# Kernel optimization log

Measured on AMD Instinct MI355X. Metric: run time of the kernel, lower is better.

Reference implementation:

```python
import jax, jax.numpy as jnp
import numpy as np

N = 100_000      # nodes
E = 1_600_000    # edges
G = 256          # graphs in batch
FIN = 128


def setup_inputs() -> dict:
    key = jax.random.key(0)
    ks = jax.random.split(key, 12)
    inp = {
        "x": jax.random.normal(ks[0], (N, FIN), dtype=jnp.float32),
        "edge_index": jax.random.randint(ks[1], (2, E), 0, N),
        "batch": jnp.sort(jax.random.randint(ks[2], (N,), 0, G)),
    }
    def lin(k, fi, fo):
        return jax.random.normal(k, (fi, fo), dtype=jnp.float32) / np.sqrt(fi)
    inp["W1"], inp["b1"] = lin(ks[3], 128, 128), jnp.zeros((128,), jnp.float32)
    inp["W2"], inp["b2"] = lin(ks[4], 128, 128), jnp.zeros((128,), jnp.float32)
    inp["W3"], inp["b3"] = lin(ks[5], 128, 128), jnp.zeros((128,), jnp.float32)
    inp["Wa1"], inp["ba1"] = lin(ks[6], 128, 64), jnp.zeros((64,), jnp.float32)
    inp["Wa2"], inp["ba2"] = lin(ks[7], 64, 32), jnp.zeros((32,), jnp.float32)
    inp["Wa3"], inp["ba3"] = lin(ks[8], 32, 1), jnp.zeros((1,), jnp.float32)
    inp["Wm1"], inp["bm1"] = lin(ks[9], 128, 128), jnp.zeros((128,), jnp.float32)
    inp["Wm2"], inp["bm2"] = lin(ks[10], 128, 256), jnp.zeros((256,), jnp.float32)
    return inp


def _gcn_norm(edge_index, n):
    # PyG gcn_norm with added self-loops: D^{-1/2}(A+I)D^{-1/2}
    loops = jnp.arange(n)
    row = jnp.concatenate([edge_index[0], loops])
    col = jnp.concatenate([edge_index[1], loops])
    deg = jax.ops.segment_sum(jnp.ones_like(col, dtype=jnp.float32), col, n)
    dinv = jnp.where(deg > 0, jax.lax.rsqrt(jnp.maximum(deg, 1.0)), 0.0)
    return row, col, dinv[row] * dinv[col]


def _gcn(x, row, col, norm, W, b, n):
    h = x @ W                                   # linear first, then propagate
    out = jax.ops.segment_sum(h[row] * norm[:, None], col, n)
    return out + b


def _seg_softmax(w, batch, g):
    m = jax.ops.segment_max(w, batch, g)        # [G, 1]
    m = jnp.where(jnp.isfinite(m), m, 0.0)      # guard empty segments
    e = jnp.exp(w - m[batch])
    s = jax.ops.segment_sum(e, batch, g)
    return e / (s[batch] + 1e-16)


def reference(x, edge_index, batch, W1, b1, W2, b2, W3, b3,
              Wa1, ba1, Wa2, ba2, Wa3, ba3, Wm1, bm1, Wm2, bm2):
    n = x.shape[0]
    row, col, norm = _gcn_norm(edge_index, n)
    x = jax.nn.relu(_gcn(x, row, col, norm, W1, b1, n))
    x = jax.nn.relu(_gcn(x, row, col, norm, W2, b2, n))
    x = jax.nn.relu(_gcn(x, row, col, norm, W3, b3, n))
    w = jax.nn.relu(_gcn(x, row, col, norm, Wa1, ba1, n))
    w = jax.nn.relu(_gcn(w, row, col, norm, Wa2, ba2, n))
    w = jax.nn.relu(_gcn(w, row, col, norm, Wa3, ba3, n))  # [N, 1]
    w = _seg_softmax(w, batch, G)
    pooled = jax.ops.segment_sum(x * w, batch, G)           # [G, 128]
    h = jax.nn.relu(pooled @ Wm1 + bm1)
    return h @ Wm2 + bm2                                    # [G, 256]
```

## Files before the change

### kernel.cpp

```cpp
#include <hip/hip_runtime.h>
#include <hip/hip_bf16.h>

struct f4 { float x, y, z, w; };
__device__ __forceinline__ f4 ld4(const float* p) { return *(const f4*)p; }
__device__ __forceinline__ void st4(float* p, f4 v) { *(f4*)p = v; }
__device__ __forceinline__ void acc4(f4& a, f4 b) { a.x += b.x; a.y += b.y; a.z += b.z; a.w += b.w; }


__global__ void count_kernel(const int* __restrict__ col, int* __restrict__ cnt, int E) {
    int e = blockIdx.x * 256 + threadIdx.x;
    if (e < E) atomicAdd(&cnt[col[e]], 1);
}


__global__ void scan1_kernel(const int* __restrict__ cnt, int* __restrict__ bsum, int n) {
    __shared__ int red[256];
    int t = threadIdx.x;
    int i = blockIdx.x * 256 + t;
    red[t] = (i < n) ? cnt[i] : 0;
    __syncthreads();
    for (int off = 128; off > 0; off >>= 1) {
        if (t < off) red[t] += red[t + off];
        __syncthreads();
    }
    if (t == 0) bsum[blockIdx.x] = red[0];
}

__global__ void scan2_kernel(int* __restrict__ bsum, int nb) {
    __shared__ int s[1024];
    int t = threadIdx.x;
    int v = (t < nb) ? bsum[t] : 0;
    s[t] = v;
    __syncthreads();
    for (int off = 1; off < 1024; off <<= 1) {
        int u = (t >= off) ? s[t - off] : 0;
        __syncthreads();
        s[t] += u;
        __syncthreads();
    }
    if (t < nb) bsum[t] = s[t] - v;
}

__global__ void scan3_kernel(const int* __restrict__ cnt, const int* __restrict__ bsum,
                             int* __restrict__ ptr, int n) {
    __shared__ int s[256];
    int t = threadIdx.x;
    int i = blockIdx.x * 256 + t;
    int v = (i < n) ? cnt[i] : 0;
    s[t] = v;
    __syncthreads();
    for (int off = 1; off < 256; off <<= 1) {
        int u = (t >= off) ? s[t - off] : 0;
        __syncthreads();
        s[t] += u;
        __syncthreads();
    }
    int excl = s[t] - v + bsum[blockIdx.x];
    if (i < n) ptr[i] = excl;
    if (i == n - 1) ptr[n] = excl + v;
}

__global__ void dinv_fill_kernel(const int* __restrict__ cnt, const int* __restrict__ ptr,
                                 float* __restrict__ dinv, int* __restrict__ fillp, int n) {
    int i = blockIdx.x * 256 + threadIdx.x;
    if (i >= n) return;
    dinv[i] = rsqrtf((float)(cnt[i] + 1));
    fillp[i] = ptr[i];
}

__global__ void fill_kernel(const int* __restrict__ row, const int* __restrict__ col,
                            int* __restrict__ fillp, int* __restrict__ csr_row, int E) {
    int e = blockIdx.x * 256 + threadIdx.x;
    if (e >= E) return;
    int c = col[e];
    int pos = atomicAdd(&fillp[c], 1);
    csr_row[pos] = row[e];
}


template<int K, int FOUT>
__global__ __launch_bounds__(256) void gemm_kernel(const float* __restrict__ A,
                            const float* __restrict__ W, const float* __restrict__ scale,
                            float* __restrict__ C, int n) {
    constexpr int ROWS = 64;
    constexpr int NCG = FOUT / 4;
    constexpr int RG  = 256 / NCG;
    constexpr int RPT = ROWS / RG;
    __shared__ float As[ROWS * K];
    int t = threadIdx.x;
    int r0 = blockIdx.x * ROWS;
    for (int i = t; i < ROWS * K / 4; i += 256) {
        int idx = i * 4;
        int r = r0 + idx / K;
        f4 v;
        if (r < n) v = ld4(A + (size_t)r0 * K + idx);
        else { v.x = v.y = v.z = v.w = 0.f; }
        st4(As + idx, v);
    }
    __syncthreads();
    int cg = t % NCG, rg = t / NCG;
    int c = cg * 4, rb = rg * RPT;
    f4 acc[RPT];
#pragma unroll
    for (int i = 0; i < RPT; ++i) { acc[i].x = acc[i].y = acc[i].z = acc[i].w = 0.f; }
    for (int k = 0; k < K; k += 4) {
        f4 w0 = ld4(W + (size_t)(k + 0) * FOUT + c);
        f4 w1 = ld4(W + (size_t)(k + 1) * FOUT + c);
        f4 w2 = ld4(W + (size_t)(k + 2) * FOUT + c);
        f4 w3 = ld4(W + (size_t)(k + 3) * FOUT + c);
#pragma unroll
        for (int i = 0; i < RPT; ++i) {
            f4 a = ld4(As + (rb + i) * K + k);
            acc[i].x += a.x * w0.x + a.y * w1.x + a.z * w2.x + a.w * w3.x;
            acc[i].y += a.x * w0.y + a.y * w1.y + a.z * w2.y + a.w * w3.y;
            acc[i].z += a.x * w0.z + a.y * w1.z + a.z * w2.z + a.w * w3.z;
            acc[i].w += a.x * w0.w + a.y * w1.w + a.z * w2.w + a.w * w3.w;
        }
    }
#pragma unroll
    for (int i = 0; i < RPT; ++i) {
        int r = r0 + rb + i;
        if (r < n) {
            float s = scale[r];
            f4 v = acc[i];
            v.x *= s; v.y *= s; v.z *= s; v.w *= s;
            st4(C + (size_t)r * FOUT + c, v);
        }
    }
}

__global__ void dot32_kernel(const float* __restrict__ A, const float* __restrict__ W,
                             const float* __restrict__ dinv, float* __restrict__ out, int n) {
    int i = blockIdx.x * 256 + threadIdx.x;
    if (i >= n) return;
    float acc = 0.f;
#pragma unroll
    for (int k = 0; k < 32; k += 4) {
        f4 a = ld4(A + (size_t)i * 32 + k);
        f4 w = ld4(W + k);
        acc += a.x * w.x + a.y * w.y + a.z * w.z + a.w * w.w;
    }
    out[i] = acc * dinv[i];
}


template<int F>
__global__ __launch_bounds__(256) void prop_kernel(const float* __restrict__ Hs,
                            const int* __restrict__ ptr, const int* __restrict__ rows,
                            const float* __restrict__ dinv, const float* __restrict__ bias,
                            float* __restrict__ out, int n) {
    constexpr int L = F / 4;
    constexpr int NPB = 256 / L;
    int t = threadIdx.x;
    int q = t % L;
    int ln = t / L;
    int node = blockIdx.x * NPB + ln;
    if (node >= n) return;
    const int f4i = q * 4;
    f4 a0 = ld4(Hs + (size_t)node * F + f4i);
    f4 a1, a2, a3;
    a1.x=a1.y=a1.z=a1.w=0.f; a2=a1; a3=a1;
    int e0 = ptr[node], e1 = ptr[node + 1];
    int e = e0;
    for (; e + 4 <= e1; e += 4) {
        int r0 = rows[e], r1 = rows[e+1], r2 = rows[e+2], r3 = rows[e+3];
        acc4(a0, ld4(Hs + (size_t)r0 * F + f4i));
        acc4(a1, ld4(Hs + (size_t)r1 * F + f4i));
        acc4(a2, ld4(Hs + (size_t)r2 * F + f4i));
        acc4(a3, ld4(Hs + (size_t)r3 * F + f4i));
    }
    for (; e < e1; ++e) acc4(a0, ld4(Hs + (size_t)rows[e] * F + f4i));
    acc4(a0, a1); acc4(a2, a3); acc4(a0, a2);
    float dn = dinv[node];
    f4 b = ld4(bias + f4i);
    f4 v;
    v.x = a0.x * dn + b.x; v.y = a0.y * dn + b.y;
    v.z = a0.z * dn + b.z; v.w = a0.w * dn + b.w;
    v.x = v.x > 0.f ? v.x : 0.f; v.y = v.y > 0.f ? v.y : 0.f;
    v.z = v.z > 0.f ? v.z : 0.f; v.w = v.w > 0.f ? v.w : 0.f;
    st4(out + (size_t)node * F + f4i, v);
}

__global__ void prop1_kernel(const float* __restrict__ Hs, const int* __restrict__ ptr,
                             const int* __restrict__ rows, const float* __restrict__ dinv,
                             const float* __restrict__ bias, float* __restrict__ out, int n) {
    int node = blockIdx.x * 256 + threadIdx.x;
    if (node >= n) return;
    float a0 = Hs[node], a1 = 0.f, a2 = 0.f, a3 = 0.f;
    int e0 = ptr[node], e1 = ptr[node + 1];
    int e = e0;
    for (; e + 4 <= e1; e += 4) {
        a0 += Hs[rows[e]];
        a1 += Hs[rows[e+1]];
        a2 += Hs[rows[e+2]];
        a3 += Hs[rows[e+3]];
    }
    for (; e < e1; ++e) a0 += Hs[rows[e]];
    float v = (a0 + a1 + a2 + a3) * dinv[node] + bias[0];
    out[node] = v > 0.f ? v : 0.f;
}


__global__ void bounds_kernel(const int* __restrict__ batch, int* __restrict__ start,
                              int n, int g_cnt) {
    int g = blockIdx.x * 256 + threadIdx.x;
    if (g > g_cnt) return;
    if (g == g_cnt) { start[g] = n; return; }
    int lo = 0, hi = n;
    while (lo < hi) { int mid = (lo + hi) >> 1; if (batch[mid] < g) lo = mid + 1; else hi = mid; }
    start[g] = lo;
}

__global__ __launch_bounds__(256) void softpool_kernel(const float* __restrict__ x,
                              const float* __restrict__ w, const int* __restrict__ start,
                              float* __restrict__ pooled) {
    int g = blockIdx.x;
    int s = start[g], e = start[g + 1];
    int t = threadIdx.x;
    __shared__ float red[256];
    float mx = -1e30f;
    for (int i = s + t; i < e; i += 256) mx = fmaxf(mx, w[i]);
    red[t] = mx; __syncthreads();
    for (int off = 128; off > 0; off >>= 1) {
        if (t < off) red[t] = fmaxf(red[t], red[t + off]);
        __syncthreads();
    }
    float m = (e > s) ? red[0] : 0.f;
    __syncthreads();
    float sm = 0.f;
    for (int i = s + t; i < e; i += 256) sm += expf(w[i] - m);
    red[t] = sm; __syncthreads();
    for (int off = 128; off > 0; off >>= 1) {
        if (t < off) red[t] += red[t + off];
        __syncthreads();
    }
    float denom = red[0] + 1e-16f;
    __syncthreads();
    int f = t & 127;
    int half = t >> 7;
    float acc = 0.f;
    for (int i = s + half; i < e; i += 2)
        acc += x[(size_t)i * 128 + f] * (expf(w[i] - m) / denom);
    red[t] = acc; __syncthreads();
    if (half == 0) pooled[g * 128 + f] = red[f] + red[128 + f];
}


__global__ void mlp1_kernel(const float* __restrict__ pooled, const float* __restrict__ Wm1,
                            const float* __restrict__ bm1, float* __restrict__ hidden) {
    int g = blockIdx.x, j = threadIdx.x;
    __shared__ float p[128];
    p[j] = pooled[g * 128 + j];
    __syncthreads();
    float acc = bm1[j];
    for (int k = 0; k < 128; ++k) acc += p[k] * Wm1[k * 128 + j];
    hidden[g * 128 + j] = acc > 0.f ? acc : 0.f;
}

__global__ void mlp2_kernel(const float* __restrict__ hidden, const float* __restrict__ Wm2,
                            const float* __restrict__ bm2, float* __restrict__ out) {
    int g = blockIdx.x, j = threadIdx.x;
    __shared__ float h[128];
    if (j < 128) h[j] = hidden[g * 128 + j];
    __syncthreads();
    float acc = bm2[j];
    for (int k = 0; k < 128; ++k) acc += h[k] * Wm2[k * 256 + j];
    out[g * 256 + j] = acc;
}


extern "C" void kernel_launch(void* const* d_in, const int* in_sizes, int n_in,
                              void* d_out, int out_size, void* d_ws, size_t ws_size,
                              hipStream_t stream) {
    const float* x    = (const float*)d_in[0];
    const int*   ei   = (const int*)d_in[1];
    const int*   batch= (const int*)d_in[2];
    const float* W1 = (const float*)d_in[3];  const float* b1 = (const float*)d_in[4];
    const float* W2 = (const float*)d_in[5];  const float* b2 = (const float*)d_in[6];
    const float* W3 = (const float*)d_in[7];  const float* b3 = (const float*)d_in[8];
    const float* Wa1= (const float*)d_in[9];  const float* ba1= (const float*)d_in[10];
    const float* Wa2= (const float*)d_in[11]; const float* ba2= (const float*)d_in[12];
    const float* Wa3= (const float*)d_in[13]; const float* ba3= (const float*)d_in[14];
    const float* Wm1= (const float*)d_in[15]; const float* bm1= (const float*)d_in[16];
    const float* Wm2= (const float*)d_in[17]; const float* bm2= (const float*)d_in[18];
    float* out = (float*)d_out;

    const int N = in_sizes[0] / 128;
    const int E = in_sizes[1] / 2;
    const int G = out_size / 256;

    const int* row = ei;
    const int* col = ei + E;

    char* wp = (char*)d_ws;
    auto alloc = [&](size_t bytes) {
        void* p = wp;
        wp += (bytes + 255) & ~(size_t)255;
        return p;
    };
    const int NB256 = (N + 255) / 256;
    int*   cnt     = (int*)alloc((size_t)N * 4);
    int*   ptr     = (int*)alloc((size_t)(N + 1) * 4);
    int*   bsum    = (int*)alloc((size_t)NB256 * 4);
    int*   fillp   = (int*)alloc((size_t)N * 4);
    int*   csr_row = (int*)alloc((size_t)E * 4);
    float* dinv    = (float*)alloc((size_t)N * 4);
    float* bufA    = (float*)alloc((size_t)N * 128 * 4);
    float* bufB    = (float*)alloc((size_t)N * 128 * 4);
    float* wb0     = (float*)alloc((size_t)N * 4);
    float* wb1     = (float*)alloc((size_t)N * 4);
    int*   gstart  = (int*)alloc((size_t)(G + 1) * 4);
    float* pooled  = (float*)alloc((size_t)G * 128 * 4);
    float* hidden  = (float*)alloc((size_t)G * 128 * 4);

    hipMemsetAsync(cnt, 0, (size_t)N * 4, stream);

    const int EB = (E + 255) / 256;
    const int NB = NB256;

    count_kernel<<<EB, 256, 0, stream>>>(col, cnt, E);
    scan1_kernel<<<NB, 256, 0, stream>>>(cnt, bsum, N);
    scan2_kernel<<<1, 1024, 0, stream>>>(bsum, NB);
    scan3_kernel<<<NB, 256, 0, stream>>>(cnt, bsum, ptr, N);
    dinv_fill_kernel<<<NB, 256, 0, stream>>>(cnt, ptr, dinv, fillp, N);
    fill_kernel<<<EB, 256, 0, stream>>>(row, col, fillp, csr_row, E);
    bounds_kernel<<<(G + 256) / 256, 256, 0, stream>>>(batch, gstart, N, G);

    const int GB64 = (N + 63) / 64;

    gemm_kernel<128,128><<<GB64, 256, 0, stream>>>(x,    W1, dinv, bufA, N);
    prop_kernel<128><<<(N + 7) / 8, 256, 0, stream>>>(bufA, ptr, csr_row, dinv, b1, bufB, N);
    gemm_kernel<128,128><<<GB64, 256, 0, stream>>>(bufB, W2, dinv, bufA, N);
    prop_kernel<128><<<(N + 7) / 8, 256, 0, stream>>>(bufA, ptr, csr_row, dinv, b2, bufB, N);
    gemm_kernel<128,128><<<GB64, 256, 0, stream>>>(bufB, W3, dinv, bufA, N);
    prop_kernel<128><<<(N + 7) / 8, 256, 0, stream>>>(bufA, ptr, csr_row, dinv, b3, bufB, N);

    float* a64_lin = bufA;
    float* a64     = bufA + (size_t)N * 64;
    gemm_kernel<128,64><<<GB64, 256, 0, stream>>>(bufB, Wa1, dinv, a64_lin, N);
    prop_kernel<64><<<(N + 15) / 16, 256, 0, stream>>>(a64_lin, ptr, csr_row, dinv, ba1, a64, N);

    float* a32_lin = bufA;
    float* a32     = bufA + (size_t)N * 32;
    gemm_kernel<64,32><<<GB64, 256, 0, stream>>>(a64, Wa2, dinv, a32_lin, N);
    prop_kernel<32><<<(N + 31) / 32, 256, 0, stream>>>(a32_lin, ptr, csr_row, dinv, ba2, a32, N);

    dot32_kernel<<<NB, 256, 0, stream>>>(a32, Wa3, dinv, wb0, N);
    prop1_kernel<<<NB, 256, 0, stream>>>(wb0, ptr, csr_row, dinv, ba3, wb1, N);

    softpool_kernel<<<G, 256, 0, stream>>>(bufB, wb1, gstart, pooled);

    mlp1_kernel<<<G, 128, 0, stream>>>(pooled, Wm1, bm1, hidden);
    mlp2_kernel<<<G, 256, 0, stream>>>(hidden, Wm2, bm2, out);
}
```

Before: 1.103 ms.

## Fuse GCN propagation with next layer's GEMM and vectorize CSR build

Adds a propgemm kernel that gathers neighbor rows, applies bias, ReLU and degree scaling into shared memory, then multiplies by the next layer's weight in the same block. This avoids writing and re-reading the intermediate activations for layers 1→2, 2→3 and a1→a2. A propdot kernel similarly fuses the 32-wide propagation with the final dot product. Count and fill kernels now process four edges per thread with int4 loads. Fusion reduces occupancy, since gather latency is no longer overlapped across as many blocks, and the 64-row tiles lose the finer per-node parallelism of the separate propagation kernel.

```diff
diff --git a/kernel.cpp b/kernel.cpp
--- a/kernel.cpp
+++ b/kernel.cpp
@@ -8,8 +8,17 @@
 
 
 __global__ void count_kernel(const int* __restrict__ col, int* __restrict__ cnt, int E) {
-    int e = blockIdx.x * 256 + threadIdx.x;
-    if (e < E) atomicAdd(&cnt[col[e]], 1);
+    int i = blockIdx.x * 256 + threadIdx.x;
+    int e0 = i * 4;
+    if (e0 + 4 <= E) {
+        int4 c = *(const int4*)(col + e0);
+        atomicAdd(&cnt[c.x], 1);
+        atomicAdd(&cnt[c.y], 1);
+        atomicAdd(&cnt[c.z], 1);
+        atomicAdd(&cnt[c.w], 1);
+    } else {
+        for (int e = e0; e < E; ++e) atomicAdd(&cnt[col[e]], 1);
+    }
 }
 
 
@@ -70,11 +79,22 @@
 
 __global__ void fill_kernel(const int* __restrict__ row, const int* __restrict__ col,
                             int* __restrict__ fillp, int* __restrict__ csr_row, int E) {
-    int e = blockIdx.x * 256 + threadIdx.x;
-    if (e >= E) return;
-    int c = col[e];
-    int pos = atomicAdd(&fillp[c], 1);
-    csr_row[pos] = row[e];
+    int i = blockIdx.x * 256 + threadIdx.x;
+    int e0 = i * 4;
+    if (e0 + 4 <= E) {
+        int4 c = *(const int4*)(col + e0);
+        int4 r = *(const int4*)(row + e0);
+        int p0 = atomicAdd(&fillp[c.x], 1);
+        int p1 = atomicAdd(&fillp[c.y], 1);
+        int p2 = atomicAdd(&fillp[c.z], 1);
+        int p3 = atomicAdd(&fillp[c.w], 1);
+        csr_row[p0] = r.x; csr_row[p1] = r.y; csr_row[p2] = r.z; csr_row[p3] = r.w;
+    } else {
+        for (int e = e0; e < E; ++e) {
+            int p = atomicAdd(&fillp[col[e]], 1);
+            csr_row[p] = row[e];
+        }
+    }
 }
 
 
@@ -129,18 +149,123 @@
     }
 }
 
-__global__ void dot32_kernel(const float* __restrict__ A, const float* __restrict__ W,
-                             const float* __restrict__ dinv, float* __restrict__ out, int n) {
-    int i = blockIdx.x * 256 + threadIdx.x;
-    if (i >= n) return;
-    float acc = 0.f;
-#pragma unroll
-    for (int k = 0; k < 32; k += 4) {
-        f4 a = ld4(A + (size_t)i * 32 + k);
-        f4 w = ld4(W + k);
-        acc += a.x * w.x + a.y * w.y + a.z * w.z + a.w * w.w;
-    }
-    out[i] = acc * dinv[i];
+
+template<int K, int FOUT, bool WRITE_AGG>
+__global__ __launch_bounds__(256) void propgemm_kernel(const float* __restrict__ Hs,
+                            const int* __restrict__ ptr, const int* __restrict__ rows,
+                            const float* __restrict__ dinv, const float* __restrict__ bias,
+                            const float* __restrict__ W, float* __restrict__ aggout,
+                            float* __restrict__ C, int n) {
+    constexpr int ROWS = 64;
+    __shared__ float As[ROWS * K];
+    int t = threadIdx.x;
+    int r0 = blockIdx.x * ROWS;
+
+    constexpr int L = K / 4;
+    constexpr int NPB = 256 / L;
+    int q = t % L, ln = t / L;
+    const int f4i = q * 4;
+    for (int p = 0; p < ROWS; p += NPB) {
+        int node = r0 + p + ln;
+        f4 a0;
+        if (node < n) {
+            a0 = ld4(Hs + (size_t)node * K + f4i);
+            f4 a1, a2, a3;
+            a1.x = a1.y = a1.z = a1.w = 0.f; a2 = a1; a3 = a1;
+            int e0 = ptr[node], e1 = ptr[node + 1];
+            int e = e0;
+            for (; e + 4 <= e1; e += 4) {
+                int rr0 = rows[e], rr1 = rows[e+1], rr2 = rows[e+2], rr3 = rows[e+3];
+                acc4(a0, ld4(Hs + (size_t)rr0 * K + f4i));
+                acc4(a1, ld4(Hs + (size_t)rr1 * K + f4i));
+                acc4(a2, ld4(Hs + (size_t)rr2 * K + f4i));
+                acc4(a3, ld4(Hs + (size_t)rr3 * K + f4i));
+            }
+            for (; e < e1; ++e) acc4(a0, ld4(Hs + (size_t)rows[e] * K + f4i));
+            acc4(a0, a1); acc4(a2, a3); acc4(a0, a2);
+            float dn = dinv[node];
+            f4 b = ld4(bias + f4i);
+            a0.x = fmaxf(a0.x * dn + b.x, 0.f);
+            a0.y = fmaxf(a0.y * dn + b.y, 0.f);
+            a0.z = fmaxf(a0.z * dn + b.z, 0.f);
+            a0.w = fmaxf(a0.w * dn + b.w, 0.f);
+            if (WRITE_AGG) st4(aggout + (size_t)node * K + f4i, a0);
+        } else { a0.x = a0.y = a0.z = a0.w = 0.f; }
+        st4(As + (p + ln) * K + f4i, a0);
+    }
+    __syncthreads();
+
+    constexpr int NCG = FOUT / 4;
+    constexpr int RG  = 256 / NCG;
+    constexpr int RPT = ROWS / RG;
+    int cg = t % NCG, rg = t / NCG;
+    int c = cg * 4, rb = rg * RPT;
+    f4 acc[RPT];
+#pragma unroll
+    for (int i = 0; i < RPT; ++i) { acc[i].x = acc[i].y = acc[i].z = acc[i].w = 0.f; }
+    for (int k = 0; k < K; k += 4) {
+        f4 w0 = ld4(W + (size_t)(k + 0) * FOUT + c);
+        f4 w1 = ld4(W + (size_t)(k + 1) * FOUT + c);
+        f4 w2 = ld4(W + (size_t)(k + 2) * FOUT + c);
+        f4 w3 = ld4(W + (size_t)(k + 3) * FOUT + c);
+#pragma unroll
+        for (int i = 0; i < RPT; ++i) {
+            f4 a = ld4(As + (rb + i) * K + k);
+            acc[i].x += a.x * w0.x + a.y * w1.x + a.z * w2.x + a.w * w3.x;
+            acc[i].y += a.x * w0.y + a.y * w1.y + a.z * w2.y + a.w * w3.y;
+            acc[i].z += a.x * w0.z + a.y * w1.z + a.z * w2.z + a.w * w3.z;
+            acc[i].w += a.x * w0.w + a.y * w1.w + a.z * w2.w + a.w * w3.w;
+        }
+    }
+#pragma unroll
+    for (int i = 0; i < RPT; ++i) {
+        int r = r0 + rb + i;
+        if (r < n) {
+            float s = dinv[r];
+            f4 v = acc[i];
+            v.x *= s; v.y *= s; v.z *= s; v.w *= s;
+            st4(C + (size_t)r * FOUT + c, v);
+        }
+    }
+}
+
+
+__global__ __launch_bounds__(256) void propdot_kernel(const float* __restrict__ Hs,
+                            const int* __restrict__ ptr, const int* __restrict__ rows,
+                            const float* __restrict__ dinv, const float* __restrict__ bias,
+                            const float* __restrict__ W, float* __restrict__ outv, int n) {
+    int t = threadIdx.x;
+    int q = t & 7;
+    int ln = t >> 3;
+    int node = blockIdx.x * 32 + ln;
+    if (node >= n) return;
+    const int f4i = q * 4;
+    f4 a0 = ld4(Hs + (size_t)node * 32 + f4i);
+    f4 a1, a2, a3;
+    a1.x = a1.y = a1.z = a1.w = 0.f; a2 = a1; a3 = a1;
+    int e0 = ptr[node], e1 = ptr[node + 1];
+    int e = e0;
+    for (; e + 4 <= e1; e += 4) {
+        int rr0 = rows[e], rr1 = rows[e+1], rr2 = rows[e+2], rr3 = rows[e+3];
+        acc4(a0, ld4(Hs + (size_t)rr0 * 32 + f4i));
+        acc4(a1, ld4(Hs + (size_t)rr1 * 32 + f4i));
+        acc4(a2, ld4(Hs + (size_t)rr2 * 32 + f4i));
+        acc4(a3, ld4(Hs + (size_t)rr3 * 32 + f4i));
+    }
+    for (; e < e1; ++e) acc4(a0, ld4(Hs + (size_t)rows[e] * 32 + f4i));
+    acc4(a0, a1); acc4(a2, a3); acc4(a0, a2);
+    float dn = dinv[node];
+    f4 b = ld4(bias + f4i);
+    float vx = fmaxf(a0.x * dn + b.x, 0.f);
+    float vy = fmaxf(a0.y * dn + b.y, 0.f);
+    float vz = fmaxf(a0.z * dn + b.z, 0.f);
+    float vw = fmaxf(a0.w * dn + b.w, 0.f);
+    f4 w = ld4(W + f4i);
+    float part = vx * w.x + vy * w.y + vz * w.z + vw * w.w;
+    part += __shfl_down(part, 4, 8);
+    part += __shfl_down(part, 2, 8);
+    part += __shfl_down(part, 1, 8);
+    if (q == 0) outv[node] = part * dn;
 }
 
 
@@ -159,7 +284,7 @@
     const int f4i = q * 4;
     f4 a0 = ld4(Hs + (size_t)node * F + f4i);
     f4 a1, a2, a3;
-    a1.x=a1.y=a1.z=a1.w=0.f; a2=a1; a3=a1;
+    a1.x = a1.y = a1.z = a1.w = 0.f; a2 = a1; a3 = a1;
     int e0 = ptr[node], e1 = ptr[node + 1];
     int e = e0;
     for (; e + 4 <= e1; e += 4) {
@@ -315,37 +440,29 @@
 
     hipMemsetAsync(cnt, 0, (size_t)N * 4, stream);
 
-    const int EB = (E + 255) / 256;
+    const int E4B = ((E + 3) / 4 + 255) / 256;
     const int NB = NB256;
 
-    count_kernel<<<EB, 256, 0, stream>>>(col, cnt, E);
+    count_kernel<<<E4B, 256, 0, stream>>>(col, cnt, E);
     scan1_kernel<<<NB, 256, 0, stream>>>(cnt, bsum, N);
     scan2_kernel<<<1, 1024, 0, stream>>>(bsum, NB);
     scan3_kernel<<<NB, 256, 0, stream>>>(cnt, bsum, ptr, N);
     dinv_fill_kernel<<<NB, 256, 0, stream>>>(cnt, ptr, dinv, fillp, N);
-    fill_kernel<<<EB, 256, 0, stream>>>(row, col, fillp, csr_row, E);
+    fill_kernel<<<E4B, 256, 0, stream>>>(row, col, fillp, csr_row, E);
     bounds_kernel<<<(G + 256) / 256, 256, 0, stream>>>(batch, gstart, N, G);
 
     const int GB64 = (N + 63) / 64;
 
-    gemm_kernel<128,128><<<GB64, 256, 0, stream>>>(x,    W1, dinv, bufA, N);
-    prop_kernel<128><<<(N + 7) / 8, 256, 0, stream>>>(bufA, ptr, csr_row, dinv, b1, bufB, N);
-    gemm_kernel<128,128><<<GB64, 256, 0, stream>>>(bufB, W2, dinv, bufA, N);
-    prop_kernel<128><<<(N + 7) / 8, 256, 0, stream>>>(bufA, ptr, csr_row, dinv, b2, bufB, N);
-    gemm_kernel<128,128><<<GB64, 256, 0, stream>>>(bufB, W3, dinv, bufA, N);
+    gemm_kernel<128,128><<<GB64, 256, 0, stream>>>(x, W1, dinv, bufA, N);
+    propgemm_kernel<128,128,false><<<GB64, 256, 0, stream>>>(bufA, ptr, csr_row, dinv, b1, W2, nullptr, bufB, N);
+    propgemm_kernel<128,128,false><<<GB64, 256, 0, stream>>>(bufB, ptr, csr_row, dinv, b2, W3, nullptr, bufA, N);
     prop_kernel<128><<<(N + 7) / 8, 256, 0, stream>>>(bufA, ptr, csr_row, dinv, b3, bufB, N);
 
     float* a64_lin = bufA;
-    float* a64     = bufA + (size_t)N * 64;
+    float* a32_lin = bufA + (size_t)N * 64;
     gemm_kernel<128,64><<<GB64, 256, 0, stream>>>(bufB, Wa1, dinv, a64_lin, N);
-    prop_kernel<64><<<(N + 15) / 16, 256, 0, stream>>>(a64_lin, ptr, csr_row, dinv, ba1, a64, N);
-
-    float* a32_lin = bufA;
-    float* a32     = bufA + (size_t)N * 32;
-    gemm_kernel<64,32><<<GB64, 256, 0, stream>>>(a64, Wa2, dinv, a32_lin, N);
-    prop_kernel<32><<<(N + 31) / 32, 256, 0, stream>>>(a32_lin, ptr, csr_row, dinv, ba2, a32, N);
-
-    dot32_kernel<<<NB, 256, 0, stream>>>(a32, Wa3, dinv, wb0, N);
+    propgemm_kernel<64,32,false><<<GB64, 256, 0, stream>>>(a64_lin, ptr, csr_row, dinv, ba1, Wa2, nullptr, a32_lin, N);
+    propdot_kernel<<<(N + 31) / 32, 256, 0, stream>>>(a32_lin, ptr, csr_row, dinv, ba2, Wa3, wb0, N);
     prop1_kernel<<<NB, 256, 0, stream>>>(wb0, ptr, csr_row, dinv, ba3, wb1, N);
 
     softpool_kernel<<<G, 256, 0, stream>>>(bufB, wb1, gstart, pooled);
```

Result: slower. 1.129 ms (+2.4%).
